# Kernel optimization log

Hardware: AMD Instinct MI355X
Metric: run time of the kernel (lower is better)

The kernel has to match this reference:

```python
import jax, jax.numpy as jnp
import numpy as np

HEADS = 20


def cape_embed(f, P):
    # f: [b, s, d], P: [b, s, 4, 4]; rotate channel groups of 4 by P
    b, s, d = f.shape
    f4 = f.reshape(b, s, d // 4, 4)
    out = jnp.einsum('bsik,bskj->bsij', f4, P)
    return out.reshape(b, s, d)


def setup_inputs() -> dict:
    key = jax.random.key(0)
    ks = jax.random.split(key, 9)
    bt, l, d = 2, 1024, 1280  # (b*t_out, tokens, channels)
    t_out, b = 2, 1
    sd = 1.0 / np.sqrt(d)
    return {
        'hidden_states': jax.random.normal(ks[0], (bt, l, d), jnp.float32),
        'p_out': jax.random.normal(ks[1], (b, t_out, 4, 4), jnp.float32) * 0.5,
        'p_out_inv': jax.random.normal(ks[2], (b, t_out, 4, 4), jnp.float32) * 0.5,
        'Wq': jax.random.normal(ks[3], (d, d), jnp.float32) * sd,
        'Wk': jax.random.normal(ks[4], (d, d), jnp.float32) * sd,
        'Wv': jax.random.normal(ks[5], (d, d), jnp.float32) * sd,
        'Wo': jax.random.normal(ks[6], (d, d), jnp.float32) * sd,
        'bo': jnp.zeros((d,), jnp.float32),
    }


def reference(hidden_states, p_out, p_out_inv, Wq, Wk, Wv, Wo, bo):
    residual = hidden_states  # [(b t_out), l, d]
    b = p_out.shape[0]
    t_out = p_out.shape[1]
    bt, l, d = hidden_states.shape
    s = t_out * l
    hd = d // HEADS
    scale = hd ** -0.5

    # rearrange '(b t_out) l d -> b (t_out l) d'
    hs = hidden_states.reshape(b, s, d)

    q = hs @ Wq
    k = hs @ Wk
    v = hs @ Wv

    # repeat per-frame CAPE matrices over spatial tokens: 'b t f g -> b (t l) f g'
    Pq = jnp.repeat(p_out_inv, l, axis=1)  # [b, s, 4, 4]
    Pk = jnp.repeat(p_out, l, axis=1)      # self-attn: p_in := p_out
    q = cape_embed(q, Pq)
    k = cape_embed(k, Pk)

    # head split: [b, s, d] -> [b, h, s, hd]
    qh = q.reshape(b, s, HEADS, hd).transpose(0, 2, 1, 3)
    kh = k.reshape(b, s, HEADS, hd).transpose(0, 2, 1, 3)
    vh = v.reshape(b, s, HEADS, hd).transpose(0, 2, 1, 3)

    scores = jnp.einsum('bhsd,bhtd->bhst', qh, kh) * scale
    probs = jax.nn.softmax(scores, axis=-1)
    out = jnp.einsum('bhst,bhtd->bhsd', probs, vh)

    out = out.transpose(0, 2, 1, 3).reshape(b, s, d)
    out = out @ Wo + bo

    # rearrange 'b (t_out l) d -> (b t_out) l d'
    out = out.reshape(bt, l, d)
    out = out + residual  # residual_connection; rescale_output_factor = 1.0
    return out
```

## Files before the change

kernel.cpp:

```cpp
#include <hip/hip_runtime.h>

typedef short short8 __attribute__((ext_vector_type(8)));
typedef short short4v __attribute__((ext_vector_type(4)));
typedef float f32x4 __attribute__((ext_vector_type(4)));
typedef float float4v __attribute__((ext_vector_type(4)));
typedef __bf16 bf16x8 __attribute__((ext_vector_type(8)));
typedef _Float16 half4 __attribute__((ext_vector_type(4)));
typedef _Float16 half2v __attribute__((ext_vector_type(2)));

__device__ __forceinline__ short f2bf(float x) {
  unsigned u = __builtin_bit_cast(unsigned, x);
  u += 0x7fffu + ((u >> 16) & 1u);
  return (short)(u >> 16);
}

__device__ __forceinline__ f32x4 mfma16(short8 a, short8 b, f32x4 c) {
  return __builtin_amdgcn_mfma_f32_16x16x32_bf16(
      __builtin_bit_cast(bf16x8, a), __builtin_bit_cast(bf16x8, b), c, 0, 0, 0);
}

__device__ __forceinline__ void async16(void* lds, const void* g) {
  __builtin_amdgcn_global_load_lds(
      (const __attribute__((address_space(1))) unsigned*)g,
      (__attribute__((address_space(3))) unsigned*)lds, 16, 0, 0);
}

__global__ __launch_bounds__(256) void capeT_all_kernel(
    const float* __restrict__ Wq, const float* __restrict__ Wk,
    const float* __restrict__ Wv, const float* __restrict__ Wo,
    const float* __restrict__ p_inv, const float* __restrict__ p_out,
    float qscale, short* __restrict__ BT0, short* __restrict__ BT1,
    short* __restrict__ wo_t, const float* __restrict__ hs,
    short* __restrict__ hs_bf) {
  const int ND = 1280, KD = 1280;
  const size_t SEC = (size_t)1280 * 1280;
  int z = blockIdx.z;
  int tx = threadIdx.x, ty = threadIdx.y;
  if (z == 4) {
    int t = ty * 32 + tx;
    int base = ((blockIdx.y * 40 + blockIdx.x) * 256 + t) * 2;
    const int n4 = 2048 * 1280 / 4;
#pragma unroll
    for (int r = 0; r < 2; r++) {
      int i = base + r;
      if (i < n4) {
        float4v v = *(const float4v*)(hs + (size_t)i * 4);
        short4v o;
#pragma unroll
        for (int j = 0; j < 4; j++) o[j] = f2bf(v[j]);
        *(short4v*)(hs_bf + (size_t)i * 4) = o;
      }
    }
    return;
  }
  const float* W;
  const float* P;
  float scale = 1.0f;
  short *d0, *d1;
  if (z == 0) { W = Wq; P = p_inv; scale = qscale; d0 = BT0; d1 = BT1; }
  else if (z == 1) { W = Wk; P = p_out; d0 = BT0 + SEC; d1 = BT1 + SEC; }
  else if (z == 2) { W = Wv; P = nullptr; d0 = BT0 + 2 * SEC; d1 = BT1 + 2 * SEC; }
  else { W = Wo; P = nullptr; d0 = wo_t; d1 = nullptr; }

  __shared__ float tile[32][33];
  int bn = blockIdx.x * 32, bk = blockIdx.y * 32;
  for (int i = ty; i < 32; i += 8)
    tile[i][tx] = W[(size_t)(bk + i) * ND + bn + tx];
  __syncthreads();
  for (int c = ty; c < 32; c += 8) {
    float v0, v1;
    if (P) {
      int g = c & ~3, jj = c & 3;
      float a0 = 0.f, a1 = 0.f;
#pragma unroll
      for (int j = 0; j < 4; j++) {
        float wv = tile[tx][g + j];
        a0 += wv * P[j * 4 + jj];
        a1 += wv * P[16 + j * 4 + jj];
      }
      v0 = a0 * scale;
      v1 = a1 * scale;
    } else {
      v0 = v1 = tile[tx][c] * scale;
    }
    size_t o = (size_t)(bn + c) * KD + bk + tx;
    d0[o] = f2bf(v0);
    if (d1) d1[o] = f2bf(v1);
  }
}


__global__ __launch_bounds__(256) void gemm128_qkv_kernel(
    const short* __restrict__ A, const short* __restrict__ B0,
    const short* __restrict__ B1, int M, int N, int K,
    short* __restrict__ qb, short* __restrict__ ktl,
    _Float16* __restrict__ vtl) {
  __shared__ __align__(16) short As[2][128][32];
  __shared__ __align__(16) short Bs[2][128][32];
  int tid = threadIdx.x;
  int l = tid & 63, w = tid >> 6;
  int wr = w >> 1, wc = w & 1;
  int lr = l & 15, lg = l >> 4;
  int nwg = gridDim.x * gridDim.y;
  int orig = blockIdx.y * gridDim.x + blockIdx.x;
  int wgid = (orig & 7) * (nwg >> 3) + (orig >> 3);
  int bxs = wgid % gridDim.x, bys = wgid / gridDim.x;
  int bm = bys * 128, bn = bxs * 128;
  const short* BT = (bm >= 1024) ? B1 : B0;
  f32x4 acc[4][4] = {};

  auto stage = [&](int b, int k0) {
    const short* ga = A + (size_t)(bm + (tid >> 2)) * K + k0 + (tid & 3) * 8;
    const short* gb = BT + (size_t)(bn + (tid >> 2)) * K + k0 + (tid & 3) * 8;
    char* la = (char*)&As[b][0][0] + w * 1024;
    char* lb = (char*)&Bs[b][0][0] + w * 1024;
    async16(la, ga);
    async16(la + 4096, ga + (size_t)64 * K);
    async16(lb, gb);
    async16(lb + 4096, gb + (size_t)64 * K);
  };

  auto compute = [&](int b) {
    const short* Ab = &As[b][0][0];
    const short* Bb = &Bs[b][0][0];
    short8 af[4], bf_[4];
#pragma unroll
    for (int mi = 0; mi < 4; mi++)
      af[mi] = *(const short8*)(Ab + (wr * 64 + mi * 16 + lr) * 32 + lg * 8);
#pragma unroll
    for (int nj = 0; nj < 4; nj++)
      bf_[nj] = *(const short8*)(Bb + (wc * 64 + nj * 16 + lr) * 32 + lg * 8);
#pragma unroll
    for (int mi = 0; mi < 4; mi++)
#pragma unroll
      for (int nj = 0; nj < 4; nj++)
        acc[mi][nj] = mfma16(af[mi], bf_[nj], acc[mi][nj]);
  };

  int nk = K >> 5;
  stage(0, 0);
  for (int ks = 0; ks < nk; ks += 2) {
    __syncthreads();
    if (ks + 1 < nk) stage(1, (ks + 1) << 5);
    compute(0);
    __syncthreads();
    if (ks + 2 < nk) stage(0, (ks + 2) << 5);
    compute(1);
  }

#pragma unroll
  for (int mi = 0; mi < 4; mi++)
#pragma unroll
    for (int nj = 0; nj < 4; nj++) {
      int s0 = bm + wr * 64 + mi * 16 + lg * 4;
      int col = bn + wc * 64 + nj * 16 + lr;
      if (col < 1280) {
#pragma unroll
        for (int i = 0; i < 4; i++)
          qb[(((size_t)(col >> 6)) * 2048 + s0 + i) * 64 + (col & 63)] =
              f2bf(acc[mi][nj][i]);
      } else if (col < 2560) {
        int cc = col - 1280;
        int h = cc >> 6, d = cc & 63;
#pragma unroll
        for (int i = 0; i < 4; i++) {
          int s = s0 + i;
          int kt = s >> 6, r = s & 63;
          int kcol = (((d >> 3) ^ (r & 7)) << 3) | (d & 7);
          ktl[(((size_t)h * 32 + kt) * 64 + r) * 64 + kcol] = f2bf(acc[mi][nj][i]);
        }
      } else {
        int cc = col - 2560;
        int h = cc >> 6, dv = cc & 63;
        int kt = s0 >> 6, key0 = s0 & 63;
        int sub = key0 >> 5, g = (key0 & 31) >> 2;
        half4 o;
#pragma unroll
        for (int i = 0; i < 4; i++) o[i] = (_Float16)acc[mi][nj][i];
        size_t vaddr = ((size_t)h * 32 + kt) * 4096 + sub * 2048 + g * 256 +
                       ((dv ^ g) << 2);
        *(half4*)(vtl + vaddr) = o;
      }
    }
}


__global__ __launch_bounds__(256) void gemm64_o_kernel(
    const short* __restrict__ A, const short* __restrict__ BT,
    int M, int N, int K, const float* __restrict__ bias,
    const float* __restrict__ resid, float* __restrict__ out) {
  __shared__ __align__(16) short As[2][64][32];
  __shared__ __align__(16) short Bs[2][64][32];
  int tid = threadIdx.x;
  int l = tid & 63, w = tid >> 6;
  int wr = w >> 1, wc = w & 1;
  int lr = l & 15, lg = l >> 4;
  int nwg = gridDim.x * gridDim.y;
  int orig = blockIdx.y * gridDim.x + blockIdx.x;
  int wgid = (orig & 7) * (nwg >> 3) + (orig >> 3);
  int bxs = wgid % gridDim.x, bys = wgid / gridDim.x;
  int bm = bys * 64, bn = bxs * 64;
  f32x4 acc[2][2] = {};

  auto stage = [&](int b, int k0) {
    const short* ga = A + (size_t)(bm + (tid >> 2)) * K + k0 + (tid & 3) * 8;
    const short* gb = BT + (size_t)(bn + (tid >> 2)) * K + k0 + (tid & 3) * 8;
    async16((char*)&As[b][0][0] + w * 1024, ga);
    async16((char*)&Bs[b][0][0] + w * 1024, gb);
  };

  auto compute = [&](int b) {
    const short* Ab = &As[b][0][0];
    const short* Bb = &Bs[b][0][0];
    short8 af[2], bf_[2];
#pragma unroll
    for (int mi = 0; mi < 2; mi++)
      af[mi] = *(const short8*)(Ab + (wr * 32 + mi * 16 + lr) * 32 + lg * 8);
#pragma unroll
    for (int nj = 0; nj < 2; nj++)
      bf_[nj] = *(const short8*)(Bb + (wc * 32 + nj * 16 + lr) * 32 + lg * 8);
#pragma unroll
    for (int mi = 0; mi < 2; mi++)
#pragma unroll
      for (int nj = 0; nj < 2; nj++)
        acc[mi][nj] = mfma16(af[mi], bf_[nj], acc[mi][nj]);
  };

  int nk = K >> 5;
  stage(0, 0);
  for (int ks = 0; ks < nk; ks += 2) {
    __syncthreads();
    if (ks + 1 < nk) stage(1, (ks + 1) << 5);
    compute(0);
    __syncthreads();
    if (ks + 2 < nk) stage(0, (ks + 2) << 5);
    compute(1);
  }

#pragma unroll
  for (int mi = 0; mi < 2; mi++)
#pragma unroll
    for (int nj = 0; nj < 2; nj++)
#pragma unroll
      for (int i = 0; i < 4; i++) {
        int row = bm + wr * 32 + mi * 16 + lg * 4 + i;
        int col = bn + wc * 32 + nj * 16 + lr;
        out[(size_t)row * N + col] =
            acc[mi][nj][i] + bias[col] + resid[(size_t)row * N + col];
      }
}

__global__ __launch_bounds__(256) void attn_kernel(
    const short* __restrict__ qb, const short* __restrict__ k_tiled,
    const _Float16* __restrict__ v_tiled, float* __restrict__ opart,
    float2* __restrict__ ml) {
  const int S = 2048, HD = 64;
  int orig = (blockIdx.z * 32 + blockIdx.y) * 20 + blockIdx.x;
  int wgid = (orig & 7) * 160 + (orig >> 3);
  int h = wgid / 64;
  int rem = wgid - h * 64;
  int qblk = rem & 31;
  int half = rem >> 5;
  int sbase = half * 32;
  int tid = threadIdx.x;
  int w = tid >> 6, l = tid & 63;
  int lr = l & 15, lg = l >> 4;
  int q0 = qblk * 64 + w * 16;

  __shared__ __align__(16) short Kl[2][32][64];
  __shared__ __align__(16) _Float16 Vl[2][2048];

  const short* qptr = qb + ((size_t)h * S + q0 + lr) * HD;
  short8 qf0 = *(const short8*)(qptr + lg * 8);
  short8 qf1 = *(const short8*)(qptr + 32 + lg * 8);

  auto stageKV = [&](int b, int ts) {
    int kt = ts >> 1, sub = ts & 1;
    const short* gk = k_tiled + ((size_t)h * 32 + kt) * 4096 + sub * 2048 + tid * 8;
    const _Float16* gv = v_tiled + ((size_t)h * 32 + kt) * 4096 + sub * 2048 + tid * 8;
    async16((char*)&Kl[b][0][0] + w * 1024, gk);
    async16((char*)&Vl[b][0] + w * 1024, gv);
  };

  float m = -1e30f, lsum = 0.f;
  f32x4 oacc[4] = {};

  auto compute_tile = [&](int buf) {
    const short* Kb = &Kl[buf][0][0];
    const _Float16* Vb = &Vl[buf][0];
    f32x4 st[2];
    __builtin_amdgcn_s_setprio(1);
#pragma unroll
    for (int kk = 0; kk < 2; kk++) {
      int r = kk * 16 + lr;
      int sw = r & 7;
      short8 kf0 = *(const short8*)(Kb + r * 64 + ((lg ^ sw) << 3));
      short8 kf1 = *(const short8*)(Kb + r * 64 + (((4 + lg) ^ sw) << 3));
      f32x4 s0 = {};
      s0 = mfma16(kf0, qf0, s0);
      s0 = mfma16(kf1, qf1, s0);
      st[kk] = s0;
    }
    __builtin_amdgcn_s_setprio(0);
    float m0 = fmaxf(fmaxf(st[0][0], st[0][1]), fmaxf(st[0][2], st[0][3]));
    float m1 = fmaxf(fmaxf(st[1][0], st[1][1]), fmaxf(st[1][2], st[1][3]));
    float pmax = fmaxf(m0, m1);
    if (!__all(pmax <= m + 8.0f)) {
      float tm = pmax;
      tm = fmaxf(tm, __shfl_xor(tm, 16));
      tm = fmaxf(tm, __shfl_xor(tm, 32));
      float mnew = fmaxf(m, tm);
      float fac = __builtin_amdgcn_exp2f(m - mnew);
      lsum *= fac;
#pragma unroll
      for (int i = 0; i < 4; i++) {
        float fi = __shfl(fac, lg * 4 + i);
#pragma unroll
        for (int nb = 0; nb < 4; nb++) oacc[nb][i] *= fi;
      }
      m = mnew;
    }
    half4 pf[2];
    float ps[2];
#pragma unroll
    for (int kk = 0; kk < 2; kk++) {
      float p0 = __builtin_amdgcn_exp2f(st[kk][0] - m);
      float p1 = __builtin_amdgcn_exp2f(st[kk][1] - m);
      float p2 = __builtin_amdgcn_exp2f(st[kk][2] - m);
      float p3 = __builtin_amdgcn_exp2f(st[kk][3] - m);
      half2v lo = __builtin_bit_cast(half2v, __builtin_amdgcn_cvt_pkrtz(p0, p1));
      half2v hi = __builtin_bit_cast(half2v, __builtin_amdgcn_cvt_pkrtz(p2, p3));
      pf[kk][0] = lo[0]; pf[kk][1] = lo[1];
      pf[kk][2] = hi[0]; pf[kk][3] = hi[1];
      ps[kk] = (p0 + p1) + (p2 + p3);
    }
    lsum += ps[0] + ps[1];
#pragma unroll
    for (int kk = 0; kk < 2; kk++) {
      half4 vf[4];
#pragma unroll
      for (int nb = 0; nb < 4; nb++) {
        int dv = nb * 16 + lr;
        int g = (kk << 2) + lg;
        vf[nb] = *(const half4*)(Vb + (g << 8) + ((dv ^ g) << 2));
      }
      __builtin_amdgcn_s_setprio(1);
#pragma unroll
      for (int nb = 0; nb < 4; nb++)
        oacc[nb] = __builtin_amdgcn_mfma_f32_16x16x16f16(pf[kk], vf[nb], oacc[nb], 0, 0, 0);
      __builtin_amdgcn_s_setprio(0);
    }
  };

  stageKV(0, sbase);
  for (int t2 = 0; t2 < 32; t2 += 2) {
    __syncthreads();
    if (t2 + 1 < 32) stageKV(1, sbase + t2 + 1);
    compute_tile(0);
    __syncthreads();
    if (t2 + 2 < 32) stageKV(0, sbase + t2 + 2);
    compute_tile(1);
  }

  lsum += __shfl_xor(lsum, 16);
  lsum += __shfl_xor(lsum, 32);

  size_t blk = (size_t)half * 640 + h * 32 + qblk;
  float* obase = opart + blk * 4096;
#pragma unroll
  for (int i = 0; i < 4; i++) {
    int ql = w * 16 + lg * 4 + i;
#pragma unroll
    for (int nb = 0; nb < 4; nb++)
      obase[ql * 64 + nb * 16 + lr] = oacc[nb][i];
  }
  if (lg == 0) {
    float2 v;
    v.x = m;
    v.y = lsum;
    ml[blk * 64 + w * 16 + lr] = v;
  }
}

__global__ __launch_bounds__(256) void attn_combine_kernel(
    const float* __restrict__ opart, const float2* __restrict__ ml,
    short* __restrict__ attn_out) {
  int h = blockIdx.x, qb = blockIdx.y;
  int t = threadIdx.x;
  int ql = t >> 2, dq = (t & 3) * 16;
  size_t blk = (size_t)h * 32 + qb;
  float2 ml0 = ml[blk * 64 + ql];
  float2 ml1 = ml[(size_t)640 * 64 + blk * 64 + ql];
  float M = fmaxf(ml0.x, ml1.x);
  float a0 = __builtin_amdgcn_exp2f(ml0.x - M);
  float a1 = __builtin_amdgcn_exp2f(ml1.x - M);
  float inv = 1.0f / (ml0.y * a0 + ml1.y * a1);
  float s0 = a0 * inv, s1 = a1 * inv;
  const float* o0 = opart + blk * 4096 + ql * 64 + dq;
  const float* o1 = o0 + (size_t)640 * 4096;
  int row = qb * 64 + ql;
  short* dst = attn_out + (size_t)row * 1280 + h * 64 + dq;
#pragma unroll
  for (int d = 0; d < 16; d += 4) {
    float4v v0 = *(const float4v*)(o0 + d);
    float4v v1 = *(const float4v*)(o1 + d);
    short4v o;
#pragma unroll
    for (int j = 0; j < 4; j++) o[j] = f2bf(v0[j] * s0 + v1[j] * s1);
    *(short4v*)(dst + d) = o;
  }
}


extern "C" void kernel_launch(void* const* d_in, const int* in_sizes, int n_in,
                              void* d_out, int out_size, void* d_ws, size_t ws_size,
                              hipStream_t stream) {
  const float* hs = (const float*)d_in[0];
  const float* p_out = (const float*)d_in[1];
  const float* p_inv = (const float*)d_in[2];
  const float* Wq = (const float*)d_in[3];
  const float* Wk = (const float*)d_in[4];
  const float* Wv = (const float*)d_in[5];
  const float* Wo = (const float*)d_in[6];
  const float* bo = (const float*)d_in[7];
  float* out = (float*)d_out;
  char* ws = (char*)d_ws;

  short* hs_bf = (short*)(ws + 0);
  short* BT0 = (short*)(ws + 5242880);
  short* BT1 = (short*)(ws + 15073280);
  short* wo_t = (short*)(ws + 24903680);
  short* q_bf = (short*)(ws + 28180480);
  short* k_tiled = (short*)(ws + 33423360);
  _Float16* v_tiled = (_Float16*)(ws + 38666240);
  short* attn_bf = (short*)(ws + 43909120);
  float* opart = (float*)(ws + 0);
  float2* ml = (float2*)(ws + 22020096);

  const float QSCALE = 0.125f * 1.44269504f;

  capeT_all_kernel<<<dim3(40, 40, 5), dim3(32, 8), 0, stream>>>(
      Wq, Wk, Wv, Wo, p_inv, p_out, QSCALE, BT0, BT1, wo_t, hs, hs_bf);

  gemm128_qkv_kernel<<<dim3(30, 16), 256, 0, stream>>>(
      hs_bf, BT0, BT1, 2048, 3840, 1280, q_bf, k_tiled, v_tiled);

  attn_kernel<<<dim3(20, 32, 2), 256, 0, stream>>>(
      q_bf, k_tiled, v_tiled, opart, ml);

  attn_combine_kernel<<<dim3(20, 32), 256, 0, stream>>>(opart, ml, attn_bf);

  gemm64_o_kernel<<<dim3(20, 32), 256, 0, stream>>>(
      attn_bf, wo_t, 2048, 1280, 1280, bo, hs, out);
}
```

Baseline: 118.4 us.

## Fuse split-KV attention combine into the output-projection GEMM A-operand staging

Removes the separate attention combine kernel. The O-projection GEMM now builds its A tile by reading both fp32 partial attention outputs and their max/sum statistics, rescaling them, converting to bf16 and storing straight into LDS. This saves one kernel launch plus the bf16 attention-output round trip through global memory. In exchange, each 64-column block of the GEMM redoes the combine for its rows, so the fp32 partials are re-read once per column block (20 times in total). A staging also becomes synchronous register loads instead of async global-to-LDS copies, which cuts into the overlap with compute.

```diff
diff --git a/kernel.cpp b/kernel.cpp
--- a/kernel.cpp
+++ b/kernel.cpp
@@ -185,10 +185,11 @@
 }
 
 
-__global__ __launch_bounds__(256) void gemm64_o_kernel(
-    const short* __restrict__ A, const short* __restrict__ BT,
-    int M, int N, int K, const float* __restrict__ bias,
-    const float* __restrict__ resid, float* __restrict__ out) {
+__global__ __launch_bounds__(256) void gemm64_oc_kernel(
+    const float* __restrict__ opart, const float2* __restrict__ ml,
+    const short* __restrict__ BT, int M, int N, int K,
+    const float* __restrict__ bias, const float* __restrict__ resid,
+    float* __restrict__ out) {
   __shared__ __align__(16) short As[2][64][32];
   __shared__ __align__(16) short Bs[2][64][32];
   int tid = threadIdx.x;
@@ -202,10 +203,37 @@
   int bm = bys * 64, bn = bxs * 64;
   f32x4 acc[2][2] = {};
 
-  auto stage = [&](int b, int k0) {
-    const short* ga = A + (size_t)(bm + (tid >> 2)) * K + k0 + (tid & 3) * 8;
+  int arow = bm + (tid >> 2);
+  int aqb = arow >> 6, aql = arow & 63;
+
+  auto stageA = [&](int b, int k0) {
+    int c0 = k0 + (tid & 3) * 8;
+    int h = c0 >> 6, dv0 = c0 & 63;
+    size_t blk = (size_t)h * 32 + aqb;
+    const float* o0 = opart + blk * 4096 + aql * 64 + dv0;
+    const float* o1 = o0 + (size_t)640 * 4096;
+    float2 m0 = ml[blk * 64 + aql];
+    float2 m1 = ml[(size_t)640 * 64 + blk * 64 + aql];
+    float Mx = fmaxf(m0.x, m1.x);
+    float a0 = __builtin_amdgcn_exp2f(m0.x - Mx);
+    float a1 = __builtin_amdgcn_exp2f(m1.x - Mx);
+    float inv = 1.0f / (m0.y * a0 + m1.y * a1);
+    float s0 = a0 * inv, s1 = a1 * inv;
+    float4v v00 = *(const float4v*)(o0);
+    float4v v01 = *(const float4v*)(o0 + 4);
+    float4v v10 = *(const float4v*)(o1);
+    float4v v11 = *(const float4v*)(o1 + 4);
+    short8 r;
+#pragma unroll
+    for (int j = 0; j < 4; j++) {
+      r[j] = f2bf(v00[j] * s0 + v10[j] * s1);
+      r[4 + j] = f2bf(v01[j] * s0 + v11[j] * s1);
+    }
+    *(short8*)((char*)&As[b][0][0] + tid * 16) = r;
+  };
+
+  auto stageB = [&](int b, int k0) {
     const short* gb = BT + (size_t)(bn + (tid >> 2)) * K + k0 + (tid & 3) * 8;
-    async16((char*)&As[b][0][0] + w * 1024, ga);
     async16((char*)&Bs[b][0][0] + w * 1024, gb);
   };
 
@@ -227,13 +255,14 @@
   };
 
   int nk = K >> 5;
-  stage(0, 0);
+  stageB(0, 0);
+  stageA(0, 0);
   for (int ks = 0; ks < nk; ks += 2) {
     __syncthreads();
-    if (ks + 1 < nk) stage(1, (ks + 1) << 5);
+    if (ks + 1 < nk) { stageB(1, (ks + 1) << 5); stageA(1, (ks + 1) << 5); }
     compute(0);
     __syncthreads();
-    if (ks + 2 < nk) stage(0, (ks + 2) << 5);
+    if (ks + 2 < nk) { stageB(0, (ks + 2) << 5); stageA(0, (ks + 2) << 5); }
     compute(1);
   }
 
@@ -382,35 +411,6 @@
   }
 }
 
-__global__ __launch_bounds__(256) void attn_combine_kernel(
-    const float* __restrict__ opart, const float2* __restrict__ ml,
-    short* __restrict__ attn_out) {
-  int h = blockIdx.x, qb = blockIdx.y;
-  int t = threadIdx.x;
-  int ql = t >> 2, dq = (t & 3) * 16;
-  size_t blk = (size_t)h * 32 + qb;
-  float2 ml0 = ml[blk * 64 + ql];
-  float2 ml1 = ml[(size_t)640 * 64 + blk * 64 + ql];
-  float M = fmaxf(ml0.x, ml1.x);
-  float a0 = __builtin_amdgcn_exp2f(ml0.x - M);
-  float a1 = __builtin_amdgcn_exp2f(ml1.x - M);
-  float inv = 1.0f / (ml0.y * a0 + ml1.y * a1);
-  float s0 = a0 * inv, s1 = a1 * inv;
-  const float* o0 = opart + blk * 4096 + ql * 64 + dq;
-  const float* o1 = o0 + (size_t)640 * 4096;
-  int row = qb * 64 + ql;
-  short* dst = attn_out + (size_t)row * 1280 + h * 64 + dq;
-#pragma unroll
-  for (int d = 0; d < 16; d += 4) {
-    float4v v0 = *(const float4v*)(o0 + d);
-    float4v v1 = *(const float4v*)(o1 + d);
-    short4v o;
-#pragma unroll
-    for (int j = 0; j < 4; j++) o[j] = f2bf(v0[j] * s0 + v1[j] * s1);
-    *(short4v*)(dst + d) = o;
-  }
-}
-
 
 extern "C" void kernel_launch(void* const* d_in, const int* in_sizes, int n_in,
                               void* d_out, int out_size, void* d_ws, size_t ws_size,
@@ -433,7 +433,6 @@
   short* q_bf = (short*)(ws + 28180480);
   short* k_tiled = (short*)(ws + 33423360);
   _Float16* v_tiled = (_Float16*)(ws + 38666240);
-  short* attn_bf = (short*)(ws + 43909120);
   float* opart = (float*)(ws + 0);
   float2* ml = (float2*)(ws + 22020096);
 
@@ -448,8 +447,6 @@
   attn_kernel<<<dim3(20, 32, 2), 256, 0, stream>>>(
       q_bf, k_tiled, v_tiled, opart, ml);
 
-  attn_combine_kernel<<<dim3(20, 32), 256, 0, stream>>>(opart, ml, attn_bf);
-
-  gemm64_o_kernel<<<dim3(20, 32), 256, 0, stream>>>(
-      attn_bf, wo_t, 2048, 1280, 1280, bo, hs, out);
-}
+  gemm64_oc_kernel<<<dim3(20, 32), 256, 0, stream>>>(
+      opart, ml, wo_t, 2048, 1280, 1280, bo, hs, out);
+}
```

New measurement: 134.8 us. 13.8% more time.

## Store split-KV attention partials in fp16 and share V weight across frames

Applied to the files above, without the earlier changes.

Attention partial outputs are now written and read as fp16 instead of fp32, which halves the intermediate traffic between the attention and combine kernels; the combine kernel uses 8-wide vector loads and stores. The V projection no longer writes a duplicate weight copy into the second-frame buffer, and the QKV GEMM reads V columns from the first buffer for both frames. This cuts write traffic in the weight-prep kernel. The cost is reduced precision on the unnormalized partial outputs.

```diff
diff --git a/kernel.cpp b/kernel.cpp
--- a/kernel.cpp
+++ b/kernel.cpp
@@ -6,6 +6,7 @@
 typedef float float4v __attribute__((ext_vector_type(4)));
 typedef __bf16 bf16x8 __attribute__((ext_vector_type(8)));
 typedef _Float16 half4 __attribute__((ext_vector_type(4)));
+typedef _Float16 half8 __attribute__((ext_vector_type(8)));
 typedef _Float16 half2v __attribute__((ext_vector_type(2)));
 
 __device__ __forceinline__ short f2bf(float x) {
@@ -59,7 +60,7 @@
   short *d0, *d1;
   if (z == 0) { W = Wq; P = p_inv; scale = qscale; d0 = BT0; d1 = BT1; }
   else if (z == 1) { W = Wk; P = p_out; d0 = BT0 + SEC; d1 = BT1 + SEC; }
-  else if (z == 2) { W = Wv; P = nullptr; d0 = BT0 + 2 * SEC; d1 = BT1 + 2 * SEC; }
+  else if (z == 2) { W = Wv; P = nullptr; d0 = BT0 + 2 * SEC; d1 = nullptr; }
   else { W = Wo; P = nullptr; d0 = wo_t; d1 = nullptr; }
 
   __shared__ float tile[32][33];
@@ -106,7 +107,7 @@
   int wgid = (orig & 7) * (nwg >> 3) + (orig >> 3);
   int bxs = wgid % gridDim.x, bys = wgid / gridDim.x;
   int bm = bys * 128, bn = bxs * 128;
-  const short* BT = (bm >= 1024) ? B1 : B0;
+  const short* BT = (bn >= 2560) ? B0 : ((bm >= 1024) ? B1 : B0);
   f32x4 acc[4][4] = {};
 
   auto stage = [&](int b, int k0) {
@@ -252,7 +253,7 @@
 
 __global__ __launch_bounds__(256) void attn_kernel(
     const short* __restrict__ qb, const short* __restrict__ k_tiled,
-    const _Float16* __restrict__ v_tiled, float* __restrict__ opart,
+    const _Float16* __restrict__ v_tiled, _Float16* __restrict__ opart,
     float2* __restrict__ ml) {
   const int S = 2048, HD = 64;
   int orig = (blockIdx.z * 32 + blockIdx.y) * 20 + blockIdx.x;
@@ -366,13 +367,13 @@
   lsum += __shfl_xor(lsum, 32);
 
   size_t blk = (size_t)half * 640 + h * 32 + qblk;
-  float* obase = opart + blk * 4096;
+  _Float16* obase = opart + blk * 4096;
 #pragma unroll
   for (int i = 0; i < 4; i++) {
     int ql = w * 16 + lg * 4 + i;
 #pragma unroll
     for (int nb = 0; nb < 4; nb++)
-      obase[ql * 64 + nb * 16 + lr] = oacc[nb][i];
+      obase[ql * 64 + nb * 16 + lr] = (_Float16)oacc[nb][i];
   }
   if (lg == 0) {
     float2 v;
@@ -383,7 +384,7 @@
 }
 
 __global__ __launch_bounds__(256) void attn_combine_kernel(
-    const float* __restrict__ opart, const float2* __restrict__ ml,
+    const _Float16* __restrict__ opart, const float2* __restrict__ ml,
     short* __restrict__ attn_out) {
   int h = blockIdx.x, qb = blockIdx.y;
   int t = threadIdx.x;
@@ -396,18 +397,19 @@
   float a1 = __builtin_amdgcn_exp2f(ml1.x - M);
   float inv = 1.0f / (ml0.y * a0 + ml1.y * a1);
   float s0 = a0 * inv, s1 = a1 * inv;
-  const float* o0 = opart + blk * 4096 + ql * 64 + dq;
-  const float* o1 = o0 + (size_t)640 * 4096;
+  const _Float16* o0 = opart + blk * 4096 + ql * 64 + dq;
+  const _Float16* o1 = o0 + (size_t)640 * 4096;
   int row = qb * 64 + ql;
   short* dst = attn_out + (size_t)row * 1280 + h * 64 + dq;
 #pragma unroll
-  for (int d = 0; d < 16; d += 4) {
-    float4v v0 = *(const float4v*)(o0 + d);
-    float4v v1 = *(const float4v*)(o1 + d);
-    short4v o;
-#pragma unroll
-    for (int j = 0; j < 4; j++) o[j] = f2bf(v0[j] * s0 + v1[j] * s1);
-    *(short4v*)(dst + d) = o;
+  for (int d = 0; d < 16; d += 8) {
+    half8 v0 = *(const half8*)(o0 + d);
+    half8 v1 = *(const half8*)(o1 + d);
+    short8 o;
+#pragma unroll
+    for (int j = 0; j < 8; j++)
+      o[j] = f2bf((float)v0[j] * s0 + (float)v1[j] * s1);
+    *(short8*)(dst + d) = o;
   }
 }
 
@@ -434,7 +436,7 @@
   short* k_tiled = (short*)(ws + 33423360);
   _Float16* v_tiled = (_Float16*)(ws + 38666240);
   short* attn_bf = (short*)(ws + 43909120);
-  float* opart = (float*)(ws + 0);
+  _Float16* opart = (_Float16*)(ws + 0);
   float2* ml = (float2*)(ws + 22020096);
 
   const float QSCALE = 0.125f * 1.44269504f;
```

Result: faster. 115.2 us (median of 2 runs) (-2.7%).
